# Optimization experiments

Measured on AMD Instinct MI355X. Metric: run time of the kernel, lower is better.

Reference implementation:

```python
import jax, jax.numpy as jnp
import numpy as np

B, N, K = 4, 2048, 32
CQ, CK, CV = 128, 128, 256
CQ1, CK1 = max(CQ, 32), max(CK, 32)
NUM_GROUPS = 32
EPS = 1e-5


def conv1x1(x, W, b):
    # x: [B,Cin,N,K], W: [Cout,Cin], b: [Cout]
    return jnp.einsum('oc,bcnk->bonk', W, x) + b[None, :, None, None]


def group_norm(x, gamma, beta, num_groups=NUM_GROUPS, eps=EPS):
    # x: [B,C,N,K]; stats over (C//G, N, K) per group, per sample (torch GroupNorm)
    b, c, n, k = x.shape
    xg = x.reshape(b, num_groups, c // num_groups, n, k)
    mean = xg.mean(axis=(2, 3, 4), keepdims=True)
    var = xg.var(axis=(2, 3, 4), keepdims=True)
    xg = (xg - mean) * jax.lax.rsqrt(var + eps)
    x = xg.reshape(b, c, n, k)
    return x * gamma[None, :, None, None] + beta[None, :, None, None]


def setup_inputs() -> dict:
    key = jax.random.key(0)
    ks = jax.random.split(key, 24)
    nrm = lambda k, shape, s=0.05: jax.random.normal(k, shape, jnp.float32) * s
    return {
        'feat': jax.random.normal(ks[0], (B, CQ, N), jnp.float32),
        'grouped_feat': jax.random.normal(ks[1], (B, CK, N, K), jnp.float32),
        'grouped_feat_out': jax.random.normal(ks[2], (B, CV, N, K), jnp.float32),
        'count': jax.random.randint(ks[3], (B, N), 0, K + 1, jnp.int32),
        'W_fc': nrm(ks[4], (CQ1, CQ)), 'b_fc': nrm(ks[5], (CQ1,)),
        'W_gc': nrm(ks[6], (CK1, CK)), 'b_gc': nrm(ks[7], (CK1,)),
        'g1': jnp.ones((CQ1 + CK1,), jnp.float32), 'be1': jnp.zeros((CQ1 + CK1,), jnp.float32),
        'W_w1': nrm(ks[8], (CV, CQ1 + CK1)), 'b_w1': nrm(ks[9], (CV,)),
        'g2': jnp.ones((CV,), jnp.float32), 'be2': jnp.zeros((CV,), jnp.float32),
        'W_w2': nrm(ks[10], (CV, CV)), 'b_w2': nrm(ks[11], (CV,)),
        'W_fo': nrm(ks[12], (CV, CV)), 'b_fo': nrm(ks[13], (CV,)),
        'g3': jnp.ones((CV,), jnp.float32), 'be3': jnp.zeros((CV,), jnp.float32),
    }


def reference(feat, grouped_feat, grouped_feat_out, count,
              W_fc, b_fc, W_gc, b_gc, g1, be1, W_w1, b_w1,
              g2, be2, W_w2, b_w2, W_fo, b_fo, g3, be3):
    # feat_conv (1x1 on [B,CQ,N,1]) then expand along K
    feat1 = jnp.einsum('oc,bcn->bon', W_fc, feat) + b_fc[None, :, None]  # [B,CQ1,N]
    feat1 = jnp.broadcast_to(feat1[..., None], (B, CQ1, N, K))
    gfeat1 = conv1x1(grouped_feat, W_gc, b_gc)  # [B,CK1,N,K]
    total = jnp.concatenate([feat1, gfeat1], axis=1)  # [B,CQ1+CK1,N,K]

    # weight_conv: ReLU -> GN -> Conv -> ReLU -> GN -> Conv
    x = jax.nn.relu(total)
    x = group_norm(x, g1, be1)
    x = conv1x1(x, W_w1, b_w1)
    x = jax.nn.relu(x)
    x = group_norm(x, g2, be2)
    scores = conv1x1(x, W_w2, b_w2)  # [B,CV,N,K]

    # count-based neighbor mask
    cnt = jnp.clip(count, 1, None)
    mask = (jnp.arange(K, dtype=cnt.dtype) < cnt[..., None]).astype(scores.dtype)  # [B,N,K]
    mask = mask[:, None]  # [B,1,N,K]
    scores = scores * mask + (-1e9) * (1.0 - mask)
    weight = jax.nn.softmax(scores, axis=-1)

    # feat_out_conv: Conv -> GN -> ReLU
    gout = conv1x1(grouped_feat_out, W_fo, b_fo)
    gout = jax.nn.relu(group_norm(gout, g3, be3))

    return (gout * weight).sum(axis=-1)  # [B,CV,N]
```

## Files before the change

kernel.cpp:

```cpp
#include <hip/hip_runtime.h>
#include <stdint.h>

#define DEVI __device__ __forceinline__

typedef __attribute__((ext_vector_type(2))) float  f32x2;
typedef __attribute__((ext_vector_type(4))) int    i32x4;
typedef __attribute__((ext_vector_type(4))) float  f32x4;
typedef __attribute__((ext_vector_type(8))) __bf16 bf16x8;

static constexpr int BB = 4, NN = 2048, KK = 32, PP = NN * KK;
static constexpr float GEPS = 1e-5f;

DEVI unsigned short f2bf(float f) {
  unsigned u = __builtin_bit_cast(unsigned, f);
  return (unsigned short)((u + 0x7FFFu + ((u >> 16) & 1u)) >> 16);
}
DEVI float bf2f(unsigned short h) {
  unsigned u = (unsigned)h << 16;
  return __builtin_bit_cast(float, u);
}
DEVI uint2 pack4(float a, float b, float c, float d) {
  return make_uint2((unsigned)f2bf(a) | ((unsigned)f2bf(b) << 16),
                    (unsigned)f2bf(c) | ((unsigned)f2bf(d) << 16));
}
DEVI void mfma16(f32x4& d, i32x4 a, i32x4 b) {
  d = __builtin_amdgcn_mfma_f32_16x16x32_bf16(
      __builtin_bit_cast(bf16x8, a), __builtin_bit_cast(bf16x8, b), d, 0, 0, 0);
}

__global__ void prep_kern(const float* Wfc, const float* Wgc, const float* Wfo,
                          unsigned short* dWfc, unsigned short* dWgc, unsigned short* dWfo) {
  int i = blockIdx.x * 256 + threadIdx.x;
  if (i < 16384)       dWfc[i] = f2bf(Wfc[i]);
  else if (i < 32768)  dWgc[i - 16384] = f2bf(Wgc[i - 16384]);
  else if (i < 98304)  dWfo[i - 32768] = f2bf(Wfo[i - 32768]);
}

template<int CIN, int COUT, int MODE, bool RELU>
__global__ __launch_bounds__(512)
__attribute__((amdgpu_waves_per_eu(4, 4)))
void gemm_kern(const void* __restrict__ srcA, const void* __restrict__ srcB,
               const unsigned short* __restrict__ Wmat, const float* __restrict__ bias,
               unsigned short* __restrict__ out, float* __restrict__ stats, int group_base,
               int P, int tiles_per_b, int nblk) {
  constexpr int TP  = 8192 / CIN;
  constexpr int NF  = TP / 16;
  constexpr int MW  = COUT / 8;
  constexpr int MF  = MW / 16;
  constexpr int KS  = CIN / 32;
  constexpr int C8N = CIN / 8;
  __shared__ unsigned short tile[2][TP * CIN];

  const int tid = threadIdx.x;
  const int lane = tid & 63, w = tid >> 6;
  const int l15 = lane & 15, lg = lane >> 4;
  const int fr = l15 >> 1;
  const int b = blockIdx.x / nblk, blk = blockIdx.x % nblk;

  const unsigned short* Wb = (MODE == 1) ? (Wmat + (size_t)b * COUT * CIN) : Wmat;
  const float* biasb = (MODE == 1) ? (bias + b * COUT) : bias;

  i32x4 a[KS][MF];
#pragma unroll
  for (int ks = 0; ks < KS; ++ks)
#pragma unroll
    for (int mf = 0; mf < MF; ++mf)
      a[ks][mf] = *(const i32x4*)(Wb + (size_t)(w * MW + mf * 16 + l15) * CIN + ks * 32 + lg * 8);

  float ssum[MF], ssq[MF];
#pragma unroll
  for (int mf = 0; mf < MF; ++mf) { ssum[mf] = 0.f; ssq[mf] = 0.f; }

  const int pr = tid & 15;
  const int c8 = (tid >> 4) & (C8N - 1);
  const int rem = (CIN == 256) ? 0 : (tid >> 8);
  const int pbase = rem * 32 + 2 * pr;
  const float* src0 = (const float*)srcA + (size_t)b * CIN * P;
  const int sp = tid >> 4, st7 = tid & 15;
  const unsigned short* r1b = (const unsigned short*)srcA + (size_t)b * NN * 128;
  const unsigned short* r2b = (const unsigned short*)srcB + (size_t)b * PP * 128;

  f32x2 pv0[8];
  uint4 pv1[2];

  auto issue = [&](int tt) {
    if constexpr (MODE == 0) {
      const float* s = src0 + (size_t)tt * TP + pbase;
#pragma unroll
      for (int i = 0; i < 8; ++i)
        pv0[i] = *(const f32x2*)(s + (size_t)(c8 * 8 + i) * (size_t)P);
    } else {
      pv1[0] = *(const uint4*)(r1b + (size_t)tt * 128 + st7 * 8);
      pv1[1] = *(const uint4*)(r2b + ((size_t)tt * 32 + sp) * 128 + st7 * 8);
    }
  };
  auto stage = [&](int cb) {
    unsigned short* tl = tile[cb];
    if constexpr (MODE == 0) {
      const int slot = c8 ^ (pr & 7);
#pragma unroll
      for (int j = 0; j < 2; ++j) {
        uint2 lo = pack4(pv0[0][j], pv0[1][j], pv0[2][j], pv0[3][j]);
        uint2 hi = pack4(pv0[4][j], pv0[5][j], pv0[6][j], pv0[7][j]);
        *(uint4*)&tl[(pbase + j) * CIN + slot * 8] = make_uint4(lo.x, lo.y, hi.x, hi.y);
      }
    } else {
      const int f = (sp >> 1) & 7;
      *(uint4*)&tl[sp * CIN + (st7 ^ f) * 8] = pv1[0];
      *(uint4*)&tl[sp * CIN + ((16 + st7) ^ f) * 8] = pv1[1];
    }
  };

  int cb = 0;
  issue(blk);
  for (int t = blk; t < tiles_per_b; t += nblk) {
    stage(cb);
    if (t + nblk < tiles_per_b) issue(t + nblk);
    __syncthreads();

    const unsigned short* tl = tile[cb];
    const int p0 = t * TP;

    f32x4 acc[MF][NF];
#pragma unroll
    for (int mf = 0; mf < MF; ++mf)
#pragma unroll
      for (int nf = 0; nf < NF; ++nf) acc[mf][nf] = f32x4{0.f, 0.f, 0.f, 0.f};

#pragma unroll
    for (int ks = 0; ks < KS; ++ks) {
      i32x4 b4[NF];
#pragma unroll
      for (int nf = 0; nf < NF; ++nf) {
        const int row = nf * 16 + l15;
        b4[nf] = *(const i32x4*)&tl[row * CIN + ((ks * 4 + lg) ^ fr) * 8];
      }
#pragma unroll
      for (int mf = 0; mf < MF; ++mf)
#pragma unroll
        for (int nf = 0; nf < NF; ++nf) mfma16(acc[mf][nf], a[ks][mf], b4[nf]);
    }

#pragma unroll
    for (int mf = 0; mf < MF; ++mf) {
      const int o4 = w * MW + mf * 16 + lg * 4;
      const f32x4 bi = *(const f32x4*)(biasb + o4);
#pragma unroll
      for (int nf = 0; nf < NF; ++nf) {
        const int p = p0 + nf * 16 + l15;
        float y0 = acc[mf][nf][0] + bi[0];
        float y1 = acc[mf][nf][1] + bi[1];
        float y2 = acc[mf][nf][2] + bi[2];
        float y3 = acc[mf][nf][3] + bi[3];
        if (RELU) {
          y0 = fmaxf(y0, 0.f); y1 = fmaxf(y1, 0.f);
          y2 = fmaxf(y2, 0.f); y3 = fmaxf(y3, 0.f);
        }
        ssum[mf] += y0 + y1 + y2 + y3;
        ssq[mf] += y0 * y0 + y1 * y1 + y2 * y2 + y3 * y3;
        *(uint2*)(out + ((size_t)b * P + p) * COUT + o4) = pack4(y0, y1, y2, y3);
      }
    }
    cb ^= 1;
  }

#pragma unroll
  for (int mf = 0; mf < MF; ++mf) {
    float s = ssum[mf], q = ssq[mf];
#pragma unroll
    for (int d = 1; d < 16; d <<= 1) { s += __shfl_xor(s, d); q += __shfl_xor(q, d); }
    if (l15 == 0) {
      int g = group_base + ((w * MW + mf * 16 + lg * 4) >> 3);
      atomicAdd(&stats[(b * 32 + g) * 2 + 0], s);
      atomicAdd(&stats[(b * 32 + g) * 2 + 1], q);
    }
  }
}

__global__ void fold1_kern(const float* st1, const float* g1, const float* be1,
                           const float* W_w1, const float* b_w1,
                           unsigned short* W1p, float* b1p) {
  int b = blockIdx.x, tid = threadIdx.x;
  __shared__ float s_l[256], t_l[256];
  {
    int c = tid, g = c >> 3;
    float cnt = (g < 16) ? (8.f * NN) : (8.f * NN * KK);
    float su = st1[(b * 32 + g) * 2], sq = st1[(b * 32 + g) * 2 + 1];
    float mean = su / cnt;
    float var = fmaxf(sq / cnt - mean * mean, 0.f);
    float s = g1[c] * rsqrtf(var + GEPS);
    s_l[c] = s; t_l[c] = be1[c] - mean * s;
  }
  __syncthreads();
  int o = tid;
  float acc = b_w1[o];
  for (int c4 = 0; c4 < 64; ++c4) {
    float4 wv = *(const float4*)(W_w1 + o * 256 + c4 * 4);
    *(uint2*)&W1p[((size_t)b * 256 + o) * 256 + c4 * 4] =
        pack4(wv.x * s_l[c4 * 4], wv.y * s_l[c4 * 4 + 1],
              wv.z * s_l[c4 * 4 + 2], wv.w * s_l[c4 * 4 + 3]);
    acc += wv.x * t_l[c4 * 4] + wv.y * t_l[c4 * 4 + 1] +
           wv.z * t_l[c4 * 4 + 2] + wv.w * t_l[c4 * 4 + 3];
  }
  b1p[b * 256 + o] = acc;
}

__global__ void fold23_kern(const float* st2, const float* st3,
                            const float* g2, const float* be2,
                            const float* W_w2, const float* b_w2,
                            const float* g3, const float* be3,
                            unsigned short* W2p, float* b2p, float* s3t3) {
  int b = blockIdx.x, tid = threadIdx.x;
  __shared__ float s_l[256], t_l[256];
  {
    int c = tid, g = c >> 3;
    float cnt = 8.f * NN * KK;
    float su = st2[(b * 32 + g) * 2], sq = st2[(b * 32 + g) * 2 + 1];
    float mean = su / cnt;
    float var = fmaxf(sq / cnt - mean * mean, 0.f);
    float s = g2[c] * rsqrtf(var + GEPS);
    s_l[c] = s; t_l[c] = be2[c] - mean * s;

    float su3 = st3[(b * 32 + g) * 2], sq3 = st3[(b * 32 + g) * 2 + 1];
    float mean3 = su3 / cnt;
    float var3 = fmaxf(sq3 / cnt - mean3 * mean3, 0.f);
    float s3 = g3[c] * rsqrtf(var3 + GEPS);
    s3t3[(b * 256 + c) * 2 + 0] = s3;
    s3t3[(b * 256 + c) * 2 + 1] = be3[c] - mean3 * s3;
  }
  __syncthreads();
  int o = tid;
  float acc = b_w2[o];
  for (int c4 = 0; c4 < 64; ++c4) {
    float4 wv = *(const float4*)(W_w2 + o * 256 + c4 * 4);
    *(uint2*)&W2p[((size_t)b * 256 + o) * 256 + c4 * 4] =
        pack4(wv.x * s_l[c4 * 4], wv.y * s_l[c4 * 4 + 1],
              wv.z * s_l[c4 * 4 + 2], wv.w * s_l[c4 * 4 + 3]);
    acc += wv.x * t_l[c4 * 4] + wv.y * t_l[c4 * 4 + 1] +
           wv.z * t_l[c4 * 4 + 2] + wv.w * t_l[c4 * 4 + 3];
  }
  b2p[b * 256 + o] = acc;
}

__global__ __launch_bounds__(512)
__attribute__((amdgpu_waves_per_eu(4, 4)))
void k5_kern(const unsigned short* __restrict__ x2t, const unsigned short* __restrict__ gor,
             const unsigned short* __restrict__ W2p, const float* __restrict__ b2p,
             const float* __restrict__ s3t3, const int* __restrict__ count,
             float* __restrict__ out, int tiles_per_b, int nblk) {
  constexpr int GP = 264;
  __shared__ unsigned short gt[2][32 * GP];
  const int tid = threadIdx.x, lane = tid & 63, w = tid >> 6;
  const int l15 = lane & 15, lg = lane >> 4;
  const int b = blockIdx.x / nblk, blk = blockIdx.x % nblk;

  const unsigned short* Wb = W2p + (size_t)b * 65536;

  i32x4 wb[8][2];
#pragma unroll
  for (int ks = 0; ks < 8; ++ks)
#pragma unroll
    for (int of = 0; of < 2; ++of)
      wb[ks][of] = *(const i32x4*)(Wb + (size_t)(w * 32 + of * 16 + l15) * 256 + ks * 32 + lg * 8);

  float bia[2], s3v[2], t3v[2];
#pragma unroll
  for (int of = 0; of < 2; ++of) {
    int o = w * 32 + of * 16 + l15;
    bia[of] = b2p[b * 256 + o];
    s3v[of] = s3t3[(b * 256 + o) * 2 + 0];
    t3v[of] = s3t3[(b * 256 + o) * 2 + 1];
  }

  const unsigned short* xb = x2t + (size_t)b * PP * 256;
  const unsigned short* gb = gor + (size_t)b * PP * 256;

  const int sp = tid >> 4, st7 = tid & 15;
  uint4 pvg[2];
  auto issue = [&](int tt) {
    const unsigned short* g = gb + ((size_t)tt * 32 + sp) * 256;
    pvg[0] = *(const uint4*)(g + (0 + st7) * 8);
    pvg[1] = *(const uint4*)(g + (16 + st7) * 8);
  };
  auto stage = [&](int cb) {
    unsigned short* tl = gt[cb];
    const int f = (sp >> 1) & 7;
    *(uint4*)&tl[sp * GP + ((0 + st7) ^ f) * 8] = pvg[0];
    *(uint4*)&tl[sp * GP + ((16 + st7) ^ f) * 8] = pvg[1];
  };

  int cb = 0;
  issue(blk);
  for (int t = blk; t < tiles_per_b; t += nblk) {
    stage(cb);
    if (t + nblk < tiles_per_b) issue(t + nblk);
    __syncthreads();

    const unsigned short* tl = gt[cb];
    const int p0 = t * 32;

    f32x4 acc[2][2];
#pragma unroll
    for (int pf = 0; pf < 2; ++pf)
#pragma unroll
      for (int of = 0; of < 2; ++of) acc[pf][of] = f32x4{0.f, 0.f, 0.f, 0.f};

#pragma unroll
    for (int ks = 0; ks < 8; ++ks) {
      i32x4 af[2];
#pragma unroll
      for (int pf = 0; pf < 2; ++pf)
        af[pf] = *(const i32x4*)(xb + (size_t)(p0 + pf * 16 + l15) * 256 + ks * 32 + lg * 8);
#pragma unroll
      for (int pf = 0; pf < 2; ++pf)
#pragma unroll
        for (int of = 0; of < 2; ++of) mfma16(acc[pf][of], af[pf], wb[ks][of]);
    }

    const int cnt = max(count[b * NN + t], 1);
#pragma unroll
    for (int of = 0; of < 2; ++of) {
      const int o = w * 32 + of * 16 + l15;
      float sc[2][4];
#pragma unroll
      for (int pf = 0; pf < 2; ++pf)
#pragma unroll
        for (int r = 0; r < 4; ++r) {
          int k = pf * 16 + lg * 4 + r;
          float v = acc[pf][of][r] + bia[of];
          sc[pf][r] = (k < cnt) ? v : -1e9f;
        }
      float m = sc[0][0];
#pragma unroll
      for (int pf = 0; pf < 2; ++pf)
#pragma unroll
        for (int r = 0; r < 4; ++r) m = fmaxf(m, sc[pf][r]);
      m = fmaxf(m, __shfl_xor(m, 16));
      m = fmaxf(m, __shfl_xor(m, 32));
      float den = 0.f, con = 0.f;
#pragma unroll
      for (int pf = 0; pf < 2; ++pf)
#pragma unroll
        for (int r = 0; r < 4; ++r) {
          float e = __expf(sc[pf][r] - m);
          int prel = pf * 16 + lg * 4 + r;
          const int f2 = (prel >> 1) & 7;
          float g = bf2f(tl[prel * GP + (((o >> 3) ^ f2) * 8 + (o & 7))]);
          g = fmaxf(s3v[of] * g + t3v[of], 0.f);
          den += e; con += e * g;
        }
      den += __shfl_xor(den, 16); con += __shfl_xor(con, 16);
      den += __shfl_xor(den, 32); con += __shfl_xor(con, 32);
      if (lg == 0)
        out[(size_t)(b * 256 + o) * NN + t] = con / den;
    }
    cb ^= 1;
  }
}

extern "C" void kernel_launch(void* const* d_in, const int* in_sizes, int n_in,
                              void* d_out, int out_size, void* d_ws, size_t ws_size,
                              hipStream_t stream) {
  const float* feat = (const float*)d_in[0];
  const float* gf   = (const float*)d_in[1];
  const float* gfo  = (const float*)d_in[2];
  const int*   cnt  = (const int*)d_in[3];
  const float* W_fc = (const float*)d_in[4];
  const float* b_fc = (const float*)d_in[5];
  const float* W_gc = (const float*)d_in[6];
  const float* b_gc = (const float*)d_in[7];
  const float* g1   = (const float*)d_in[8];
  const float* be1  = (const float*)d_in[9];
  const float* W_w1 = (const float*)d_in[10];
  const float* b_w1 = (const float*)d_in[11];
  const float* g2   = (const float*)d_in[12];
  const float* be2  = (const float*)d_in[13];
  const float* W_w2 = (const float*)d_in[14];
  const float* b_w2 = (const float*)d_in[15];
  const float* W_fo = (const float*)d_in[16];
  const float* b_fo = (const float*)d_in[17];
  const float* g3   = (const float*)d_in[18];
  const float* be3  = (const float*)d_in[19];
  float* out = (float*)d_out;
  char* ws = (char*)d_ws;

  constexpr size_t ST1 = 0, ST2 = 1024, ST3 = 2048;
  constexpr size_t WFC = 4096;
  constexpr size_t WGC = WFC + 32768;
  constexpr size_t WFO = WGC + 32768;
  constexpr size_t W1P = WFO + 131072;
  constexpr size_t B1P = W1P + 524288;
  constexpr size_t W2P = B1P + 4096;
  constexpr size_t B2P = W2P + 524288;
  constexpr size_t S3T = B2P + 4096;
  constexpr size_t R1  = 2097152;
  constexpr size_t X2  = R1 + 2097152;
  constexpr size_t R2  = X2 + 134217728;
  constexpr size_t GOR = R2;
  constexpr size_t WS_NEED = GOR + 134217728;
  if (ws_size < WS_NEED) return;

  float* st1 = (float*)(ws + ST1);
  float* st2 = (float*)(ws + ST2);
  float* st3 = (float*)(ws + ST3);
  unsigned short* wfc = (unsigned short*)(ws + WFC);
  unsigned short* wgc = (unsigned short*)(ws + WGC);
  unsigned short* wfo = (unsigned short*)(ws + WFO);
  unsigned short* w1p = (unsigned short*)(ws + W1P);
  float* b1p = (float*)(ws + B1P);
  unsigned short* w2p = (unsigned short*)(ws + W2P);
  float* b2p = (float*)(ws + B2P);
  float* s3t = (float*)(ws + S3T);
  unsigned short* r1 = (unsigned short*)(ws + R1);
  unsigned short* x2 = (unsigned short*)(ws + X2);
  unsigned short* r2 = (unsigned short*)(ws + R2);
  unsigned short* gor = (unsigned short*)(ws + GOR);

  hipMemsetAsync(ws, 0, 3072, stream);
  prep_kern<<<384, 256, 0, stream>>>(W_fc, W_gc, W_fo, wfc, wgc, wfo);

  gemm_kern<128, 128, 0, true><<<dim3(4 * 32), 512, 0, stream>>>(
      feat, nullptr, wfc, b_fc, r1, st1, 0, NN, NN / 64, 32);
  gemm_kern<128, 128, 0, true><<<dim3(4 * 128), 512, 0, stream>>>(
      gf, nullptr, wgc, b_gc, r2, st1, 16, PP, PP / 64, 128);

  fold1_kern<<<4, 256, 0, stream>>>(st1, g1, be1, W_w1, b_w1, w1p, b1p);

  gemm_kern<256, 256, 1, true><<<dim3(4 * 128), 512, 0, stream>>>(
      r1, r2, w1p, b1p, x2, st2, 0, PP, PP / 32, 128);

  gemm_kern<256, 256, 0, false><<<dim3(4 * 128), 512, 0, stream>>>(
      gfo, nullptr, wfo, b_fo, gor, st3, 0, PP, PP / 32, 128);

  fold23_kern<<<4, 256, 0, stream>>>(st2, st3, g2, be2, W_w2, b_w2, g3, be3, w2p, b2p, s3t);

  k5_kern<<<dim3(4 * 128), 512, 0, stream>>>(x2, gor, w2p, b2p, s3t, cnt, out, PP / 32, 128);
}
```

Measured before the change: 843.2 us.

## Restructure GEMM and softmax kernels to per-wave tiles without block barriers

Result: slower. 1.455 ms (+72.6%).

```diff
diff --git a/kernel.cpp b/kernel.cpp
--- a/kernel.cpp
+++ b/kernel.cpp
@@ -3,7 +3,6 @@
 
 #define DEVI __device__ __forceinline__
 
-typedef __attribute__((ext_vector_type(2))) float  f32x2;
 typedef __attribute__((ext_vector_type(4))) int    i32x4;
 typedef __attribute__((ext_vector_type(4))) float  f32x4;
 typedef __attribute__((ext_vector_type(8))) __bf16 bf16x8;
@@ -39,26 +38,26 @@
 template<int CIN, int COUT, int MODE, bool RELU>
 __global__ __launch_bounds__(512)
 __attribute__((amdgpu_waves_per_eu(4, 4)))
-void gemm_kern(const void* __restrict__ srcA, const void* __restrict__ srcB,
-               const unsigned short* __restrict__ Wmat, const float* __restrict__ bias,
-               unsigned short* __restrict__ out, float* __restrict__ stats, int group_base,
-               int P, int tiles_per_b, int nblk) {
-  constexpr int TP  = 8192 / CIN;
-  constexpr int NF  = TP / 16;
-  constexpr int MW  = COUT / 8;
-  constexpr int MF  = MW / 16;
-  constexpr int KS  = CIN / 32;
-  constexpr int C8N = CIN / 8;
-  __shared__ unsigned short tile[2][TP * CIN];
+void wgemm_kern(const void* __restrict__ srcA, const void* __restrict__ srcB,
+                const unsigned short* __restrict__ Wmat, const float* __restrict__ bias,
+                unsigned short* __restrict__ out, float* __restrict__ stats, int group_base,
+                int P, int tiles_per_b, int nblk) {
+  constexpr int MW = (COUT == 256) ? 32 : 16;
+  constexpr int MF = MW / 16;
+  constexpr int KS = CIN / 32;
+  __shared__ unsigned short osl[8 * 16 * MW];
 
   const int tid = threadIdx.x;
   const int lane = tid & 63, w = tid >> 6;
   const int l15 = lane & 15, lg = lane >> 4;
-  const int fr = l15 >> 1;
   const int b = blockIdx.x / nblk, blk = blockIdx.x % nblk;
+  const int tpb = tiles_per_b / nblk;
 
   const unsigned short* Wb = (MODE == 1) ? (Wmat + (size_t)b * COUT * CIN) : Wmat;
   const float* biasb = (MODE == 1) ? (bias + b * COUT) : bias;
+  const float* src0 = (const float*)srcA + (size_t)b * CIN * P;
+  const unsigned short* r1b = (const unsigned short*)srcA + (size_t)b * NN * 128;
+  const unsigned short* r2b = (const unsigned short*)srcB + (size_t)b * PP * 128;
 
   i32x4 a[KS][MF];
 #pragma unroll
@@ -67,101 +66,77 @@
     for (int mf = 0; mf < MF; ++mf)
       a[ks][mf] = *(const i32x4*)(Wb + (size_t)(w * MW + mf * 16 + l15) * CIN + ks * 32 + lg * 8);
 
+  f32x4 bi[MF];
+#pragma unroll
+  for (int mf = 0; mf < MF; ++mf)
+    bi[mf] = *(const f32x4*)(biasb + w * MW + mf * 16 + lg * 4);
+
   float ssum[MF], ssq[MF];
 #pragma unroll
   for (int mf = 0; mf < MF; ++mf) { ssum[mf] = 0.f; ssq[mf] = 0.f; }
 
-  const int pr = tid & 15;
-  const int c8 = (tid >> 4) & (C8N - 1);
-  const int rem = (CIN == 256) ? 0 : (tid >> 8);
-  const int pbase = rem * 32 + 2 * pr;
-  const float* src0 = (const float*)srcA + (size_t)b * CIN * P;
-  const int sp = tid >> 4, st7 = tid & 15;
-  const unsigned short* r1b = (const unsigned short*)srcA + (size_t)b * NN * 128;
-  const unsigned short* r2b = (const unsigned short*)srcB + (size_t)b * PP * 128;
-
-  f32x2 pv0[8];
-  uint4 pv1[2];
-
-  auto issue = [&](int tt) {
-    if constexpr (MODE == 0) {
-      const float* s = src0 + (size_t)tt * TP + pbase;
-#pragma unroll
-      for (int i = 0; i < 8; ++i)
-        pv0[i] = *(const f32x2*)(s + (size_t)(c8 * 8 + i) * (size_t)P);
+  unsigned short* slice = &osl[w * 16 * MW];
+
+  for (int t = blk * tpb; t < (blk + 1) * tpb; ++t) {
+    const int p0 = t * 16;
+
+    f32x4 acc[MF];
+#pragma unroll
+    for (int mf = 0; mf < MF; ++mf) acc[mf] = f32x4{0.f, 0.f, 0.f, 0.f};
+
+#pragma unroll
+    for (int ks = 0; ks < KS; ++ks) {
+      i32x4 bf;
+      if constexpr (MODE == 0) {
+        float v[8];
+#pragma unroll
+        for (int j = 0; j < 8; ++j)
+          v[j] = src0[(size_t)(ks * 32 + lg * 8 + j) * (size_t)P + p0 + l15];
+        uint2 lo = pack4(v[0], v[1], v[2], v[3]);
+        uint2 hi = pack4(v[4], v[5], v[6], v[7]);
+        bf = i32x4{(int)lo.x, (int)lo.y, (int)hi.x, (int)hi.y};
+      } else {
+        if (ks < KS / 2) {
+          bf = *(const i32x4*)(r1b + (size_t)(p0 >> 5) * 128 + ks * 32 + lg * 8);
+        } else {
+          bf = *(const i32x4*)(r2b + (size_t)(p0 + l15) * 128 + (ks - KS / 2) * 32 + lg * 8);
+        }
+      }
+#pragma unroll
+      for (int mf = 0; mf < MF; ++mf) mfma16(acc[mf], a[ks][mf], bf);
+    }
+
+#pragma unroll
+    for (int mf = 0; mf < MF; ++mf) {
+      float y0 = acc[mf][0] + bi[mf][0];
+      float y1 = acc[mf][1] + bi[mf][1];
+      float y2 = acc[mf][2] + bi[mf][2];
+      float y3 = acc[mf][3] + bi[mf][3];
+      if (RELU) {
+        y0 = fmaxf(y0, 0.f); y1 = fmaxf(y1, 0.f);
+        y2 = fmaxf(y2, 0.f); y3 = fmaxf(y3, 0.f);
+      }
+      ssum[mf] += y0 + y1 + y2 + y3;
+      ssq[mf] += y0 * y0 + y1 * y1 + y2 * y2 + y3 * y3;
+      if constexpr (MW == 32) {
+        const int c = (mf * 4 + lg) ^ (l15 & 6);
+        *(uint2*)&slice[l15 * 32 + c * 4] = pack4(y0, y1, y2, y3);
+      } else {
+        const int c = lg ^ (l15 & 2);
+        *(uint2*)&slice[l15 * 16 + c * 4] = pack4(y0, y1, y2, y3);
+      }
+    }
+    if constexpr (MW == 32) {
+      const int pos = lane >> 2, q = lane & 3;
+      const int qs = q ^ ((pos & 6) >> 1);
+      uint4 val = *(const uint4*)&slice[pos * 32 + qs * 8];
+      *(uint4*)(out + ((size_t)b * P + p0 + pos) * COUT + w * 32 + q * 8) = val;
     } else {
-      pv1[0] = *(const uint4*)(r1b + (size_t)tt * 128 + st7 * 8);
-      pv1[1] = *(const uint4*)(r2b + ((size_t)tt * 32 + sp) * 128 + st7 * 8);
-    }
-  };
-  auto stage = [&](int cb) {
-    unsigned short* tl = tile[cb];
-    if constexpr (MODE == 0) {
-      const int slot = c8 ^ (pr & 7);
-#pragma unroll
-      for (int j = 0; j < 2; ++j) {
-        uint2 lo = pack4(pv0[0][j], pv0[1][j], pv0[2][j], pv0[3][j]);
-        uint2 hi = pack4(pv0[4][j], pv0[5][j], pv0[6][j], pv0[7][j]);
-        *(uint4*)&tl[(pbase + j) * CIN + slot * 8] = make_uint4(lo.x, lo.y, hi.x, hi.y);
-      }
-    } else {
-      const int f = (sp >> 1) & 7;
-      *(uint4*)&tl[sp * CIN + (st7 ^ f) * 8] = pv1[0];
-      *(uint4*)&tl[sp * CIN + ((16 + st7) ^ f) * 8] = pv1[1];
-    }
-  };
-
-  int cb = 0;
-  issue(blk);
-  for (int t = blk; t < tiles_per_b; t += nblk) {
-    stage(cb);
-    if (t + nblk < tiles_per_b) issue(t + nblk);
-    __syncthreads();
-
-    const unsigned short* tl = tile[cb];
-    const int p0 = t * TP;
-
-    f32x4 acc[MF][NF];
-#pragma unroll
-    for (int mf = 0; mf < MF; ++mf)
-#pragma unroll
-      for (int nf = 0; nf < NF; ++nf) acc[mf][nf] = f32x4{0.f, 0.f, 0.f, 0.f};
-
-#pragma unroll
-    for (int ks = 0; ks < KS; ++ks) {
-      i32x4 b4[NF];
-#pragma unroll
-      for (int nf = 0; nf < NF; ++nf) {
-        const int row = nf * 16 + l15;
-        b4[nf] = *(const i32x4*)&tl[row * CIN + ((ks * 4 + lg) ^ fr) * 8];
-      }
-#pragma unroll
-      for (int mf = 0; mf < MF; ++mf)
-#pragma unroll
-        for (int nf = 0; nf < NF; ++nf) mfma16(acc[mf][nf], a[ks][mf], b4[nf]);
-    }
-
-#pragma unroll
-    for (int mf = 0; mf < MF; ++mf) {
-      const int o4 = w * MW + mf * 16 + lg * 4;
-      const f32x4 bi = *(const f32x4*)(biasb + o4);
-#pragma unroll
-      for (int nf = 0; nf < NF; ++nf) {
-        const int p = p0 + nf * 16 + l15;
-        float y0 = acc[mf][nf][0] + bi[0];
-        float y1 = acc[mf][nf][1] + bi[1];
-        float y2 = acc[mf][nf][2] + bi[2];
-        float y3 = acc[mf][nf][3] + bi[3];
-        if (RELU) {
-          y0 = fmaxf(y0, 0.f); y1 = fmaxf(y1, 0.f);
-          y2 = fmaxf(y2, 0.f); y3 = fmaxf(y3, 0.f);
-        }
-        ssum[mf] += y0 + y1 + y2 + y3;
-        ssq[mf] += y0 * y0 + y1 * y1 + y2 * y2 + y3 * y3;
-        *(uint2*)(out + ((size_t)b * P + p) * COUT + o4) = pack4(y0, y1, y2, y3);
-      }
-    }
-    cb ^= 1;
+      const int pos = lane >> 2, cc = lane & 3;
+      const int cs = cc ^ (pos & 2);
+      uint2 val = *(const uint2*)&slice[pos * 16 + cs * 4];
+      *(uint2*)(out + ((size_t)b * P + p0 + pos) * COUT + w * 16 + cc * 4) = val;
+    }
   }
 
 #pragma unroll
@@ -248,11 +223,12 @@
              const unsigned short* __restrict__ W2p, const float* __restrict__ b2p,
              const float* __restrict__ s3t3, const int* __restrict__ count,
              float* __restrict__ out, int tiles_per_b, int nblk) {
-  constexpr int GP = 264;
-  __shared__ unsigned short gt[2][32 * GP];
+  __shared__ unsigned short gsl[8 * 32 * 32];
   const int tid = threadIdx.x, lane = tid & 63, w = tid >> 6;
   const int l15 = lane & 15, lg = lane >> 4;
   const int b = blockIdx.x / nblk, blk = blockIdx.x % nblk;
+  const int tpb = tiles_per_b / nblk;
+  const int wch = w * 32;
 
   const unsigned short* Wb = W2p + (size_t)b * 65536;
 
@@ -261,12 +237,12 @@
   for (int ks = 0; ks < 8; ++ks)
 #pragma unroll
     for (int of = 0; of < 2; ++of)
-      wb[ks][of] = *(const i32x4*)(Wb + (size_t)(w * 32 + of * 16 + l15) * 256 + ks * 32 + lg * 8);
+      wb[ks][of] = *(const i32x4*)(Wb + (size_t)(wch + of * 16 + l15) * 256 + ks * 32 + lg * 8);
 
   float bia[2], s3v[2], t3v[2];
 #pragma unroll
   for (int of = 0; of < 2; ++of) {
-    int o = w * 32 + of * 16 + l15;
+    int o = wch + of * 16 + l15;
     bia[of] = b2p[b * 256 + o];
     s3v[of] = s3t3[(b * 256 + o) * 2 + 0];
     t3v[of] = s3t3[(b * 256 + o) * 2 + 1];
@@ -274,30 +250,18 @@
 
   const unsigned short* xb = x2t + (size_t)b * PP * 256;
   const unsigned short* gb = gor + (size_t)b * PP * 256;
-
-  const int sp = tid >> 4, st7 = tid & 15;
-  uint4 pvg[2];
-  auto issue = [&](int tt) {
-    const unsigned short* g = gb + ((size_t)tt * 32 + sp) * 256;
-    pvg[0] = *(const uint4*)(g + (0 + st7) * 8);
-    pvg[1] = *(const uint4*)(g + (16 + st7) * 8);
-  };
-  auto stage = [&](int cb) {
-    unsigned short* tl = gt[cb];
-    const int f = (sp >> 1) & 7;
-    *(uint4*)&tl[sp * GP + ((0 + st7) ^ f) * 8] = pvg[0];
-    *(uint4*)&tl[sp * GP + ((16 + st7) ^ f) * 8] = pvg[1];
-  };
-
-  int cb = 0;
-  issue(blk);
-  for (int t = blk; t < tiles_per_b; t += nblk) {
-    stage(cb);
-    if (t + nblk < tiles_per_b) issue(t + nblk);
-    __syncthreads();
-
-    const unsigned short* tl = gt[cb];
-    const int p0 = t * 32;
+  unsigned short* slice = &gsl[w * 32 * 32];
+
+  for (int t = blk * tpb; t < (blk + 1) * tpb; ++t) {
+    const int p0 = t * 32, n = t;
+
+#pragma unroll
+    for (int h = 0; h < 2; ++h) {
+      const int pos = h * 16 + (lane >> 2), q = lane & 3;
+      uint4 gv = *(const uint4*)(gb + (size_t)(p0 + pos) * 256 + wch + q * 8);
+      const int qs = q ^ ((pos & 6) >> 1);
+      *(uint4*)&slice[pos * 32 + qs * 8] = gv;
+    }
 
     f32x4 acc[2][2];
 #pragma unroll
@@ -317,10 +281,10 @@
         for (int of = 0; of < 2; ++of) mfma16(acc[pf][of], af[pf], wb[ks][of]);
     }
 
-    const int cnt = max(count[b * NN + t], 1);
+    const int cnt = max(count[b * NN + n], 1);
 #pragma unroll
     for (int of = 0; of < 2; ++of) {
-      const int o = w * 32 + of * 16 + l15;
+      const int o = wch + of * 16 + l15;
       float sc[2][4];
 #pragma unroll
       for (int pf = 0; pf < 2; ++pf)
@@ -338,23 +302,23 @@
       m = fmaxf(m, __shfl_xor(m, 16));
       m = fmaxf(m, __shfl_xor(m, 32));
       float den = 0.f, con = 0.f;
+      const int q16 = of * 2 + (l15 >> 3);
 #pragma unroll
       for (int pf = 0; pf < 2; ++pf)
 #pragma unroll
         for (int r = 0; r < 4; ++r) {
           float e = __expf(sc[pf][r] - m);
-          int prel = pf * 16 + lg * 4 + r;
-          const int f2 = (prel >> 1) & 7;
-          float g = bf2f(tl[prel * GP + (((o >> 3) ^ f2) * 8 + (o & 7))]);
+          const int k = pf * 16 + lg * 4 + r;
+          const int qs = q16 ^ ((k & 6) >> 1);
+          float g = bf2f(slice[k * 32 + qs * 8 + (l15 & 7)]);
           g = fmaxf(s3v[of] * g + t3v[of], 0.f);
           den += e; con += e * g;
         }
       den += __shfl_xor(den, 16); con += __shfl_xor(con, 16);
       den += __shfl_xor(den, 32); con += __shfl_xor(con, 32);
       if (lg == 0)
-        out[(size_t)(b * 256 + o) * NN + t] = con / den;
-    }
-    cb ^= 1;
+        out[(size_t)(b * 256 + o) * NN + n] = con / den;
+    }
   }
 }
 
@@ -419,20 +383,20 @@
   hipMemsetAsync(ws, 0, 3072, stream);
   prep_kern<<<384, 256, 0, stream>>>(W_fc, W_gc, W_fo, wfc, wgc, wfo);
 
-  gemm_kern<128, 128, 0, true><<<dim3(4 * 32), 512, 0, stream>>>(
-      feat, nullptr, wfc, b_fc, r1, st1, 0, NN, NN / 64, 32);
-  gemm_kern<128, 128, 0, true><<<dim3(4 * 128), 512, 0, stream>>>(
-      gf, nullptr, wgc, b_gc, r2, st1, 16, PP, PP / 64, 128);
+  wgemm_kern<128, 128, 0, true><<<dim3(4 * 32), 512, 0, stream>>>(
+      feat, nullptr, wfc, b_fc, r1, st1, 0, NN, NN / 16, 32);
+  wgemm_kern<128, 128, 0, true><<<dim3(4 * 128), 512, 0, stream>>>(
+      gf, nullptr, wgc, b_gc, r2, st1, 16, PP, PP / 16, 128);
 
   fold1_kern<<<4, 256, 0, stream>>>(st1, g1, be1, W_w1, b_w1, w1p, b1p);
 
-  gemm_kern<256, 256, 1, true><<<dim3(4 * 128), 512, 0, stream>>>(
-      r1, r2, w1p, b1p, x2, st2, 0, PP, PP / 32, 128);
-
-  gemm_kern<256, 256, 0, false><<<dim3(4 * 128), 512, 0, stream>>>(
-      gfo, nullptr, wfo, b_fo, gor, st3, 0, PP, PP / 32, 128);
+  wgemm_kern<256, 256, 1, true><<<dim3(4 * 128), 512, 0, stream>>>(
+      r1, r2, w1p, b1p, x2, st2, 0, PP, PP / 16, 128);
+
+  wgemm_kern<256, 256, 0, false><<<dim3(4 * 128), 512, 0, stream>>>(
+      gfo, nullptr, wfo, b_fo, gor, st3, 0, PP, PP / 16, 128);
 
   fold23_kern<<<4, 256, 0, stream>>>(st2, st3, g2, be2, W_w2, b_w2, g3, be3, w2p, b2p, s3t);
 
-  k5_kern<<<dim3(4 * 128), 512, 0, stream>>>(x2, gor, w2p, b2p, s3t, cnt, out, PP / 32, 128);
-}
+  k5_kern<<<dim3(4 * 128), 512, 0, stream>>>(x2, gor, w2p, b2p, s3t, cnt, out, NN, 128);
+}
```
